# Optimization experiments

Hardware: AMD Instinct MI355X
Metric: run time of the kernel (lower is better)

Reference implementation:

```python
import jax, jax.numpy as jnp
import numpy as np

B, S, D = 2, 2048, 1024
H, HD = 16, 64  # head_dim = D // H
NEG = -9.0e15


def setup_inputs() -> dict:
    key = jax.random.key(0)
    ks = jax.random.split(key, 6)
    # xavier-uniform-like init for projections
    lim_qkv = float(np.sqrt(6.0 / (D + 3 * D)))
    lim_o = float(np.sqrt(6.0 / (D + D)))
    x = jax.random.normal(ks[0], (B, S, D), dtype=jnp.float32)
    qkv_w = jax.random.uniform(ks[1], (3 * D, D), minval=-lim_qkv, maxval=lim_qkv, dtype=jnp.float32)
    qkv_b = jnp.zeros((3 * D,), dtype=jnp.float32)
    o_w = jax.random.uniform(ks[2], (D, D), minval=-lim_o, maxval=lim_o, dtype=jnp.float32)
    o_b = jnp.zeros((D,), dtype=jnp.float32)
    # per-head thresholds ~ Uniform(0, 2/S): mean softmax prob is 1/S, so
    # roughly half the heads prune aggressively, half keep most entries.
    thresholds = jax.random.uniform(ks[3], (H,), dtype=jnp.float32) * (2.0 / S)
    return {"x": x, "thresholds": thresholds, "qkv_w": qkv_w, "qkv_b": qkv_b,
            "o_w": o_w, "o_b": o_b}


def reference(x, thresholds, qkv_w, qkv_b, o_w, o_b):
    # qkv projection: [B,S,3D] -> [B,S,H,3*HD] -> [B,H,S,3*HD]
    qkv = jnp.einsum('bsd,ed->bse', x, qkv_w) + qkv_b
    qkv = qkv.reshape(B, S, H, 3 * HD).transpose(0, 2, 1, 3)
    q, k, v = jnp.split(qkv, 3, axis=-1)  # each [B,H,S,HD]

    scale = 1.0 / jnp.sqrt(jnp.asarray(HD, dtype=q.dtype))
    attn_logits = jnp.einsum('bhqd,bhkd->bhqk', q, k) * scale  # [B,H,S,S]

    # first softmax only to build threshold mask (per-head threshold)
    att1 = jax.nn.softmax(attn_logits, axis=-1)
    mask = att1 > thresholds[None, :, None, None]

    # second, masked softmax
    masked_logits = jnp.where(mask, attn_logits, jnp.asarray(NEG, attn_logits.dtype))
    attention = jax.nn.softmax(masked_logits, axis=-1)

    values = jnp.einsum('bhqk,bhkd->bhqd', attention, v)  # [B,H,S,HD]
    values = values.transpose(0, 2, 1, 3).reshape(B, S, D)
    o = jnp.einsum('bsd,ed->bse', values, o_w) + o_b
    return o
```

## Files before the change

### kernel.cpp

```cpp
#include <hip/hip_runtime.h>
#include <math.h>

#define BATCH 2
#define S_LEN 2048
#define DMODEL 1024
#define NH 16
#define HDIM 64
#define SCALE 0.125f

typedef short bf16x8 __attribute__((ext_vector_type(8)));
typedef _Float16 f16x8 __attribute__((ext_vector_type(8)));
typedef float f32x4 __attribute__((ext_vector_type(4)));
typedef unsigned short u16;
typedef unsigned short u16x4 __attribute__((ext_vector_type(4)));
#define MFMA(a, b, c) __builtin_amdgcn_mfma_f32_16x16x32_bf16(a, b, c, 0, 0, 0)
#define MFMA16(a, b, c) __builtin_amdgcn_mfma_f32_16x16x32_f16(a, b, c, 0, 0, 0)

static __device__ __forceinline__ float bf2f(u16 u) {
  return __uint_as_float(((unsigned int)u) << 16);
}
static __device__ __forceinline__ u16 f2h_bits(float a) {
  _Float16 h = (_Float16)a;
  return *(u16*)&h;
}

static __device__ __forceinline__ void split_bf16(float a, u16& hi, u16& lo) {
  unsigned int u = __float_as_uint(a);
  unsigned int r = (u + 0x7fffu + ((u >> 16) & 1u)) >> 16;
  hi = (u16)r;
  float res = a - __uint_as_float(r << 16);
  unsigned int u2 = __float_as_uint(res);
  lo = (u16)((u2 + 0x7fffu + ((u2 >> 16) & 1u)) >> 16);
}

static __device__ __forceinline__ float qredsum(float v) {
#pragma unroll
  for (int off = 8; off >= 1; off >>= 1) v += __shfl_xor(v, off, 16);
  return v;
}

static __device__ __forceinline__ void async_ld16(u16* lds, const u16* g) {
  __builtin_amdgcn_global_load_lds(
      (const __attribute__((address_space(1))) void*)(const void*)g,
      (__attribute__((address_space(3))) void*)(void*)lds, 16, 0, 0);
}

__global__ __launch_bounds__(256) void split_pair_kernel(
    const float* __restrict__ in, u16* __restrict__ hi, u16* __restrict__ lo,
    int n) {
  int idx = (blockIdx.x * 256 + threadIdx.x) * 4;
  if (idx >= n) return;
  float4 v = *(const float4*)(in + idx);
  u16 h0, h1, h2, h3, l0, l1, l2, l3;
  split_bf16(v.x, h0, l0);
  split_bf16(v.y, h1, l1);
  split_bf16(v.z, h2, l2);
  split_bf16(v.w, h3, l3);
  u16x4 h = {h0, h1, h2, h3};
  u16x4 l = {l0, l1, l2, l3};
  *(u16x4*)(hi + idx) = h;
  *(u16x4*)(lo + idx) = l;
}

__global__ __launch_bounds__(256) void qkv_gemm_mfma(
    const u16* __restrict__ xh, const u16* __restrict__ xl,
    const u16* __restrict__ wh, const u16* __restrict__ wl,
    const float* __restrict__ bias, u16* __restrict__ Qhi,
    u16* __restrict__ Qlo, u16* __restrict__ Khi, u16* __restrict__ Klo,
    u16* __restrict__ Vt) {
  __shared__ __align__(16) u16 Ah[4096], Al[4096], Bh[4096], Bl[4096];
  const int tid = threadIdx.x;
  const int w = tid >> 6, lane = tid & 63;
  const int m = lane & 15, quad = lane >> 4;
  const int wm = w >> 1, wn = w & 1;
  const int m0 = blockIdx.x * 128, n0 = blockIdx.y * 128;
  const int rl = lane >> 2, bp = lane & 3;
  const int sst = (rl >> 1) & 3;
  const int sa = (quad ^ ((m >> 1) & 3)) * 8;

  f32x4 acc[4][4];
  const f32x4 vzero = {0.f, 0.f, 0.f, 0.f};
#pragma unroll
  for (int mt = 0; mt < 4; ++mt)
#pragma unroll
    for (int nt = 0; nt < 4; ++nt) acc[mt][nt] = vzero;

  for (int k0 = 0; k0 < DMODEL; k0 += 32) {
#pragma unroll
    for (int i = 0; i < 2; ++i) {
      int cc = w * 2 + i;
      int row = cc * 16 + rl;
      int gofs = k0 + ((bp ^ sst) << 3);
      async_ld16(&Ah[cc * 512], xh + (m0 + row) * DMODEL + gofs);
      async_ld16(&Al[cc * 512], xl + (m0 + row) * DMODEL + gofs);
      async_ld16(&Bh[cc * 512], wh + (n0 + row) * DMODEL + gofs);
      async_ld16(&Bl[cc * 512], wl + (n0 + row) * DMODEL + gofs);
    }
    __syncthreads();
    bf16x8 afh[4], afl[4], bfh[4], bfl[4];
#pragma unroll
    for (int t = 0; t < 4; ++t) {
      int ra = (wm * 64 + t * 16 + m) * 32 + sa;
      afh[t] = *(const bf16x8*)&Ah[ra];
      afl[t] = *(const bf16x8*)&Al[ra];
      int rb = (wn * 64 + t * 16 + m) * 32 + sa;
      bfh[t] = *(const bf16x8*)&Bh[rb];
      bfl[t] = *(const bf16x8*)&Bl[rb];
    }
#pragma unroll
    for (int mt = 0; mt < 4; ++mt)
#pragma unroll
      for (int nt = 0; nt < 4; ++nt) {
        acc[mt][nt] = MFMA(afh[mt], bfh[nt], acc[mt][nt]);
        acc[mt][nt] = MFMA(afh[mt], bfl[nt], acc[mt][nt]);
        acc[mt][nt] = MFMA(afl[mt], bfh[nt], acc[mt][nt]);
      }
    __syncthreads();
  }
#pragma unroll
  for (int mt = 0; mt < 4; ++mt) {
#pragma unroll
    for (int rg = 0; rg < 4; ++rg) {
      int grow = m0 + wm * 64 + mt * 16 + quad * 4 + rg;
      int bb = grow >> 11, s = grow & (S_LEN - 1);
#pragma unroll
      for (int nt = 0; nt < 4; ++nt) {
        int e = n0 + wn * 64 + nt * 16 + m;
        float val = acc[mt][nt][rg] + bias[e];
        int h = e / 192;
        int r = e - h * 192;
        int d = r & 63;
        int bh = bb * NH + h;
        if (r < 64) {
          u16 hi, lo;
          split_bf16(val, hi, lo);
          int off = (bh * S_LEN + s) * HDIM + d;
          Qhi[off] = hi; Qlo[off] = lo;
        } else if (r < 128) {
          u16 hi, lo;
          split_bf16(val, hi, lo);
          int off = (bh * S_LEN + s) * HDIM + d;
          Khi[off] = hi; Klo[off] = lo;
        } else {
          Vt[(bh * HDIM + d) * S_LEN + s] = f2h_bits(val);
        }
      }
    }
  }
}

__global__ __launch_bounds__(256) void o_gemm_mfma(
    const u16* __restrict__ valh, const u16* __restrict__ vall,
    const float* __restrict__ ow, const float* __restrict__ bias,
    float* __restrict__ out) {
  __shared__ __align__(16) u16 Ah[4096], Al[4096], Bh[4096], Bl[4096];
  const int tid = threadIdx.x;
  const int w = tid >> 6, lane = tid & 63;
  const int m = lane & 15, quad = lane >> 4;
  const int wm = w >> 1, wn = w & 1;
  const int m0 = blockIdx.x * 128, n0 = blockIdx.y * 128;
  const int rl = lane >> 2, bp = lane & 3;
  const int sst = (rl >> 1) & 3;
  const int sa = (quad ^ ((m >> 1) & 3)) * 8;
  const int rB = tid >> 1, hf = tid & 1;
  const int sB = (rB >> 1) & 3;

  f32x4 acc[4][4];
  const f32x4 vzero = {0.f, 0.f, 0.f, 0.f};
#pragma unroll
  for (int mt = 0; mt < 4; ++mt)
#pragma unroll
    for (int nt = 0; nt < 4; ++nt) acc[mt][nt] = vzero;

  for (int k0 = 0; k0 < DMODEL; k0 += 32) {
#pragma unroll
    for (int i = 0; i < 2; ++i) {
      int cc = w * 2 + i;
      int row = cc * 16 + rl;
      int gofs = k0 + ((bp ^ sst) << 3);
      async_ld16(&Ah[cc * 512], valh + (m0 + row) * DMODEL + gofs);
      async_ld16(&Al[cc * 512], vall + (m0 + row) * DMODEL + gofs);
    }
    {
      const float* src = ow + (n0 + rB) * DMODEL + k0 + hf * 16;
      float tmp[16];
      *(float4*)&tmp[0] = *(const float4*)(src);
      *(float4*)&tmp[4] = *(const float4*)(src + 4);
      *(float4*)&tmp[8] = *(const float4*)(src + 8);
      *(float4*)&tmp[12] = *(const float4*)(src + 12);
      u16 hbuf[16], lbuf[16];
#pragma unroll
      for (int ii = 0; ii < 16; ++ii) split_bf16(tmp[ii], hbuf[ii], lbuf[ii]);
#pragma unroll
      for (int j = 0; j < 2; ++j) {
        int bs = ((2 * hf + j) ^ sB) * 8;
        bf16x8 hv, lv;
#pragma unroll
        for (int q2 = 0; q2 < 8; ++q2) {
          hv[q2] = (short)hbuf[j * 8 + q2];
          lv[q2] = (short)lbuf[j * 8 + q2];
        }
        *(bf16x8*)&Bh[rB * 32 + bs] = hv;
        *(bf16x8*)&Bl[rB * 32 + bs] = lv;
      }
    }
    __syncthreads();
    bf16x8 afh[4], afl[4], bfh[4], bfl[4];
#pragma unroll
    for (int t = 0; t < 4; ++t) {
      int ra = (wm * 64 + t * 16 + m) * 32 + sa;
      afh[t] = *(const bf16x8*)&Ah[ra];
      afl[t] = *(const bf16x8*)&Al[ra];
      int rb = (wn * 64 + t * 16 + m) * 32 + sa;
      bfh[t] = *(const bf16x8*)&Bh[rb];
      bfl[t] = *(const bf16x8*)&Bl[rb];
    }
#pragma unroll
    for (int mt = 0; mt < 4; ++mt)
#pragma unroll
      for (int nt = 0; nt < 4; ++nt) {
        acc[mt][nt] = MFMA(afh[mt], bfh[nt], acc[mt][nt]);
        acc[mt][nt] = MFMA(afh[mt], bfl[nt], acc[mt][nt]);
        acc[mt][nt] = MFMA(afl[mt], bfh[nt], acc[mt][nt]);
      }
    __syncthreads();
  }
#pragma unroll
  for (int mt = 0; mt < 4; ++mt) {
#pragma unroll
    for (int rg = 0; rg < 4; ++rg) {
      int grow = m0 + wm * 64 + mt * 16 + quad * 4 + rg;
#pragma unroll
      for (int nt = 0; nt < 4; ++nt) {
        int e = n0 + wn * 64 + nt * 16 + m;
        out[(size_t)grow * DMODEL + e] = acc[mt][nt][rg] + bias[e];
      }
    }
  }
}

__global__ __launch_bounds__(256) void vsum_kernel(const u16* __restrict__ Vt,
                                                   float* __restrict__ vsum) {
  const int bh = blockIdx.x;
  const int tid = threadIdx.x;
  const int d = tid >> 2, part = tid & 3;
  int base = (bh * HDIM + d) * S_LEN + part * 512;
  float s = 0.f;
  for (int k = 0; k < 512; k += 8) {
    f16x8 vv = *(const f16x8*)(Vt + base + k);
#pragma unroll
    for (int j = 0; j < 8; ++j) s += (float)vv[j];
  }
  __shared__ float red[64][4];
  red[d][part] = s;
  __syncthreads();
  if (part == 0)
    vsum[bh * HDIM + d] = red[d][0] + red[d][1] + red[d][2] + red[d][3];
}

__global__ __launch_bounds__(256) void attn_mfma_kernel(
    const u16* __restrict__ Qhi, const u16* __restrict__ Qlo,
    const u16* __restrict__ Khi, const u16* __restrict__ Klo,
    const u16* __restrict__ Vt, const float* __restrict__ thr,
    const float* __restrict__ vsum, u16* __restrict__ valh,
    u16* __restrict__ vall) {
  const int blk = blockIdx.x;
  const int qt = blk & 31, bh = blk >> 5;
  const int h = bh & (NH - 1), bb = bh >> 4;
  const int tid = threadIdx.x;
  const int w = tid >> 6, lane = tid & 63;
  const int m = lane & 15, quad = lane >> 4;
  const int rsub = lane >> 3;
  const int bsw = (lane & 7) ^ rsub;

  __shared__ __align__(16) u16 Kh_s[2][4096];
  __shared__ __align__(16) u16 Kl_s[2][4096];
  __shared__ __align__(16) u16 Vs_s[4096];
  __shared__ __align__(16) u16 Pf_s[4][16][64];

  const int qoff = (bh * S_LEN + qt * 64 + w * 16 + m) * HDIM + quad * 8;
  const bf16x8 aQh0 = *(const bf16x8*)(Qhi + qoff);
  const bf16x8 aQh1 = *(const bf16x8*)(Qhi + qoff + 32);
  const bf16x8 aQl0 = *(const bf16x8*)(Qlo + qoff);
  const bf16x8 aQl1 = *(const bf16x8*)(Qlo + qoff + 32);

  const u16* KhT = Khi + bh * S_LEN * HDIM;
  const u16* KlT = Klo + bh * S_LEN * HDIM;
  const u16* VtT = Vt + bh * HDIM * S_LEN;
  const float th = thr[h];

  const int s0 = (quad ^ (m & 7)) * 8;
  const int s1 = ((4 + quad) ^ (m & 7)) * 8;

  float Zr[4], Z2r[4], tzr[4];
#pragma unroll
  for (int r = 0; r < 4; ++r) { Zr[r] = 0.f; Z2r[r] = 0.f; }

  const f32x4 vzero = {0.f, 0.f, 0.f, 0.f};

#define STAGE_K(bufi, t)                                                     \
  {                                                                          \
    const u16* gh = KhT + (t) * 64 * 64;                                     \
    const u16* gl = KlT + (t) * 64 * 64;                                     \
    _Pragma("unroll") for (int i = 0; i < 2; ++i) {                          \
      int c = w * 2 + i;                                                     \
      int row = c * 8 + rsub;                                                \
      async_ld16(&Kh_s[bufi][c * 512], gh + row * 64 + bsw * 8);             \
      async_ld16(&Kl_s[bufi][c * 512], gl + row * 64 + bsw * 8);             \
    }                                                                        \
  }
#define STAGE_V(t)                                                           \
  {                                                                          \
    _Pragma("unroll") for (int i = 0; i < 2; ++i) {                          \
      int c = w * 2 + i;                                                     \
      int row = c * 8 + rsub;                                                \
      async_ld16(&Vs_s[c * 512], VtT + row * 2048 + (t) * 64 + bsw * 8);     \
    }                                                                        \
  }

  STAGE_K(0, 0);
  __syncthreads();
  for (int t = 0; t < 32; ++t) {
    const int cur = t & 1;
    if (t < 31) STAGE_K(cur ^ 1, t + 1);
    f32x4 acc[4];
#pragma unroll
    for (int nt = 0; nt < 4; ++nt) acc[nt] = vzero;
#pragma unroll
    for (int nt = 0; nt < 4; ++nt) {
      const int ro = (nt * 16 + m) * 64;
      bf16x8 kh0 = *(const bf16x8*)&Kh_s[cur][ro + s0];
      bf16x8 kh1 = *(const bf16x8*)&Kh_s[cur][ro + s1];
      bf16x8 kl0 = *(const bf16x8*)&Kl_s[cur][ro + s0];
      bf16x8 kl1 = *(const bf16x8*)&Kl_s[cur][ro + s1];
      acc[nt] = MFMA(aQh0, kh0, acc[nt]);
      acc[nt] = MFMA(aQh1, kh1, acc[nt]);
      acc[nt] = MFMA(aQh0, kl0, acc[nt]);
      acc[nt] = MFMA(aQh1, kl1, acc[nt]);
      acc[nt] = MFMA(aQl0, kh0, acc[nt]);
      acc[nt] = MFMA(aQl1, kh1, acc[nt]);
      acc[nt] = MFMA(aQl0, kl0, acc[nt]);
      acc[nt] = MFMA(aQl1, kl1, acc[nt]);
    }
#pragma unroll
    for (int r = 0; r < 4; ++r) {
      Zr[r] += __expf(acc[0][r] * SCALE) + __expf(acc[1][r] * SCALE) +
               __expf(acc[2][r] * SCALE) + __expf(acc[3][r] * SCALE);
    }
    __syncthreads();
  }
#pragma unroll
  for (int r = 0; r < 4; ++r) tzr[r] = th * qredsum(Zr[r]);

  f32x4 oacc[4];
#pragma unroll
  for (int nt = 0; nt < 4; ++nt) oacc[nt] = vzero;

  STAGE_K(0, 0);
  __syncthreads();
  for (int t = 0; t < 32; ++t) {
    const int cur = t & 1;
    STAGE_V(t);
    if (t < 31) STAGE_K(cur ^ 1, t + 1);
    f32x4 acc[4];
#pragma unroll
    for (int nt = 0; nt < 4; ++nt) acc[nt] = vzero;
#pragma unroll
    for (int nt = 0; nt < 4; ++nt) {
      const int ro = (nt * 16 + m) * 64;
      bf16x8 kh0 = *(const bf16x8*)&Kh_s[cur][ro + s0];
      bf16x8 kh1 = *(const bf16x8*)&Kh_s[cur][ro + s1];
      bf16x8 kl0 = *(const bf16x8*)&Kl_s[cur][ro + s0];
      bf16x8 kl1 = *(const bf16x8*)&Kl_s[cur][ro + s1];
      acc[nt] = MFMA(aQh0, kh0, acc[nt]);
      acc[nt] = MFMA(aQh1, kh1, acc[nt]);
      acc[nt] = MFMA(aQh0, kl0, acc[nt]);
      acc[nt] = MFMA(aQh1, kl1, acc[nt]);
      acc[nt] = MFMA(aQl0, kh0, acc[nt]);
      acc[nt] = MFMA(aQl1, kh1, acc[nt]);
      acc[nt] = MFMA(aQl0, kl0, acc[nt]);
      acc[nt] = MFMA(aQl1, kl1, acc[nt]);
    }
#pragma unroll
    for (int r = 0; r < 4; ++r) {
      int row = quad * 4 + r;
      float psum = 0.f;
#pragma unroll
      for (int nt = 0; nt < 4; ++nt) {
        float pu = __expf(acc[nt][r] * SCALE);
        float p = (pu > tzr[r]) ? pu : 0.f;
        _Float16 p16 = (_Float16)p;
        psum += (float)p16;
        int col = nt * 16 + m;
        int cs = (((col >> 3) ^ (row & 7)) << 3) | (col & 7);
        Pf_s[w][row][cs] = *(u16*)&p16;
      }
      Z2r[r] += psum;
    }
    __syncthreads();
    f16x8 aP0 = *(const f16x8*)&Pf_s[w][m][s0];
    f16x8 aP1 = *(const f16x8*)&Pf_s[w][m][s1];
#pragma unroll
    for (int nt = 0; nt < 4; ++nt) {
      const int ro = (nt * 16 + m) * 64;
      f16x8 vv0 = *(const f16x8*)&Vs_s[ro + s0];
      f16x8 vv1 = *(const f16x8*)&Vs_s[ro + s1];
      oacc[nt] = MFMA16(aP0, vv0, oacc[nt]);
      oacc[nt] = MFMA16(aP1, vv1, oacc[nt]);
    }
    __syncthreads();
  }

#pragma unroll
  for (int r = 0; r < 4; ++r) {
    float z2 = qredsum(Z2r[r]);
    float invz = (z2 > 0.f) ? (1.f / z2) : 0.f;
    int srow = qt * 64 + w * 16 + quad * 4 + r;
#pragma unroll
    for (int nt = 0; nt < 4; ++nt) {
      float vs = vsum[bh * HDIM + nt * 16 + m];
      float o = (z2 > 0.f) ? (oacc[nt][r] * invz) : (vs * (1.0f / S_LEN));
      int idx = (bb * S_LEN + srow) * DMODEL + h * HDIM + nt * 16 + m;
      u16 hi, lo;
      split_bf16(o, hi, lo);
      valh[idx] = hi;
      vall[idx] = lo;
    }
  }
}

extern "C" void kernel_launch(void* const* d_in, const int* in_sizes, int n_in,
                              void* d_out, int out_size, void* d_ws, size_t ws_size,
                              hipStream_t stream) {
  const float* x = (const float*)d_in[0];
  const float* thresholds = (const float*)d_in[1];
  const float* qkv_w = (const float*)d_in[2];
  const float* qkv_b = (const float*)d_in[3];
  const float* o_w = (const float*)d_in[4];
  const float* o_b = (const float*)d_in[5];

  const size_t NBH = (size_t)BATCH * NH * S_LEN * HDIM;
  u16* base = (u16*)d_ws;
  u16* Qhi = base;
  u16* Qlo = base + NBH;
  u16* Khi = base + 2 * NBH;
  u16* Klo = base + 3 * NBH;
  u16* Vt = base + 4 * NBH;
  float* vsum = (float*)(base + 5 * NBH);
  u16* R1 = (u16*)(vsum + 2048);
  u16* xh = R1;
  u16* xl = R1 + NBH;
  u16* valh = R1;
  u16* vall = R1 + NBH;
  u16* wh = (u16*)d_out;
  u16* wl = wh + (size_t)3 * DMODEL * DMODEL;

  split_pair_kernel<<<4096, 256, 0, stream>>>(x, xh, xl, (int)NBH);
  split_pair_kernel<<<3072, 256, 0, stream>>>(qkv_w, wh, wl, 3 * DMODEL * DMODEL);
  dim3 g1(32, 24);
  qkv_gemm_mfma<<<g1, 256, 0, stream>>>(xh, xl, wh, wl, qkv_b, Qhi, Qlo, Khi,
                                        Klo, Vt);
  vsum_kernel<<<BATCH * NH, 256, 0, stream>>>(Vt, vsum);
  attn_mfma_kernel<<<BATCH * NH * (S_LEN / 64), 256, 0, stream>>>(
      Qhi, Qlo, Khi, Klo, Vt, thresholds, vsum, valh, vall);
  dim3 g3(32, 8);
  o_gemm_mfma<<<g3, 256, 0, stream>>>(valh, vall, o_w, o_b, (float*)d_out);
}
```

Before: 437.9 us.

## Fuse bf16 splitting into QKV GEMM, trim QK MFMAs, double-buffer V

Removes the separate hi/lo split kernels by converting x and qkv_w to bf16 pairs while staging tiles inside the QKV GEMM, sharing a helper with the output GEMM. In attention, the lo*lo QK product terms are dropped, V tiles are double-buffered and prefetched with K, and a block barrier before the P·V step is removed. exp is replaced with exp2 using a folded scale constant. This cuts kernel launches, workspace traffic and MFMA count, at the cost of synchronous loads in the GEMM staging and slightly lower QK precision.

```diff
diff --git a/kernel.cpp b/kernel.cpp
--- a/kernel.cpp
+++ b/kernel.cpp
@@ -7,12 +7,12 @@
 #define NH 16
 #define HDIM 64
 #define SCALE 0.125f
+#define KC 0.18033688011112042f
 
 typedef short bf16x8 __attribute__((ext_vector_type(8)));
 typedef _Float16 f16x8 __attribute__((ext_vector_type(8)));
 typedef float f32x4 __attribute__((ext_vector_type(4)));
 typedef unsigned short u16;
-typedef unsigned short u16x4 __attribute__((ext_vector_type(4)));
 #define MFMA(a, b, c) __builtin_amdgcn_mfma_f32_16x16x32_bf16(a, b, c, 0, 0, 0)
 #define MFMA16(a, b, c) __builtin_amdgcn_mfma_f32_16x16x32_f16(a, b, c, 0, 0, 0)
 
@@ -45,26 +45,33 @@
       (__attribute__((address_space(3))) void*)(void*)lds, 16, 0, 0);
 }
 
-__global__ __launch_bounds__(256) void split_pair_kernel(
-    const float* __restrict__ in, u16* __restrict__ hi, u16* __restrict__ lo,
-    int n) {
-  int idx = (blockIdx.x * 256 + threadIdx.x) * 4;
-  if (idx >= n) return;
-  float4 v = *(const float4*)(in + idx);
-  u16 h0, h1, h2, h3, l0, l1, l2, l3;
-  split_bf16(v.x, h0, l0);
-  split_bf16(v.y, h1, l1);
-  split_bf16(v.z, h2, l2);
-  split_bf16(v.w, h3, l3);
-  u16x4 h = {h0, h1, h2, h3};
-  u16x4 l = {l0, l1, l2, l3};
-  *(u16x4*)(hi + idx) = h;
-  *(u16x4*)(lo + idx) = l;
+static __device__ __forceinline__ void stage_split16(
+    const float* __restrict__ src, u16* __restrict__ Lh, u16* __restrict__ Ll,
+    int r, int hf, int ssw) {
+  float tmp[16];
+  *(float4*)&tmp[0] = *(const float4*)(src);
+  *(float4*)&tmp[4] = *(const float4*)(src + 4);
+  *(float4*)&tmp[8] = *(const float4*)(src + 8);
+  *(float4*)&tmp[12] = *(const float4*)(src + 12);
+  u16 hbuf[16], lbuf[16];
+#pragma unroll
+  for (int ii = 0; ii < 16; ++ii) split_bf16(tmp[ii], hbuf[ii], lbuf[ii]);
+#pragma unroll
+  for (int j = 0; j < 2; ++j) {
+    int bs = ((2 * hf + j) ^ ssw) * 8;
+    bf16x8 hv, lv;
+#pragma unroll
+    for (int q2 = 0; q2 < 8; ++q2) {
+      hv[q2] = (short)hbuf[j * 8 + q2];
+      lv[q2] = (short)lbuf[j * 8 + q2];
+    }
+    *(bf16x8*)&Lh[r * 32 + bs] = hv;
+    *(bf16x8*)&Ll[r * 32 + bs] = lv;
+  }
 }
 
 __global__ __launch_bounds__(256) void qkv_gemm_mfma(
-    const u16* __restrict__ xh, const u16* __restrict__ xl,
-    const u16* __restrict__ wh, const u16* __restrict__ wl,
+    const float* __restrict__ x, const float* __restrict__ wg,
     const float* __restrict__ bias, u16* __restrict__ Qhi,
     u16* __restrict__ Qlo, u16* __restrict__ Khi, u16* __restrict__ Klo,
     u16* __restrict__ Vt) {
@@ -74,9 +81,9 @@
   const int m = lane & 15, quad = lane >> 4;
   const int wm = w >> 1, wn = w & 1;
   const int m0 = blockIdx.x * 128, n0 = blockIdx.y * 128;
-  const int rl = lane >> 2, bp = lane & 3;
-  const int sst = (rl >> 1) & 3;
   const int sa = (quad ^ ((m >> 1) & 3)) * 8;
+  const int rS = tid >> 1, hf = tid & 1;
+  const int sS = (rS >> 1) & 3;
 
   f32x4 acc[4][4];
   const f32x4 vzero = {0.f, 0.f, 0.f, 0.f};
@@ -86,16 +93,10 @@
     for (int nt = 0; nt < 4; ++nt) acc[mt][nt] = vzero;
 
   for (int k0 = 0; k0 < DMODEL; k0 += 32) {
-#pragma unroll
-    for (int i = 0; i < 2; ++i) {
-      int cc = w * 2 + i;
-      int row = cc * 16 + rl;
-      int gofs = k0 + ((bp ^ sst) << 3);
-      async_ld16(&Ah[cc * 512], xh + (m0 + row) * DMODEL + gofs);
-      async_ld16(&Al[cc * 512], xl + (m0 + row) * DMODEL + gofs);
-      async_ld16(&Bh[cc * 512], wh + (n0 + row) * DMODEL + gofs);
-      async_ld16(&Bl[cc * 512], wl + (n0 + row) * DMODEL + gofs);
-    }
+    stage_split16(x + (size_t)(m0 + rS) * DMODEL + k0 + hf * 16, Ah, Al, rS,
+                  hf, sS);
+    stage_split16(wg + (size_t)(n0 + rS) * DMODEL + k0 + hf * 16, Bh, Bl, rS,
+                  hf, sS);
     __syncthreads();
     bf16x8 afh[4], afl[4], bfh[4], bfl[4];
 #pragma unroll
@@ -178,32 +179,11 @@
       int cc = w * 2 + i;
       int row = cc * 16 + rl;
       int gofs = k0 + ((bp ^ sst) << 3);
-      async_ld16(&Ah[cc * 512], valh + (m0 + row) * DMODEL + gofs);
-      async_ld16(&Al[cc * 512], vall + (m0 + row) * DMODEL + gofs);
-    }
-    {
-      const float* src = ow + (n0 + rB) * DMODEL + k0 + hf * 16;
-      float tmp[16];
-      *(float4*)&tmp[0] = *(const float4*)(src);
-      *(float4*)&tmp[4] = *(const float4*)(src + 4);
-      *(float4*)&tmp[8] = *(const float4*)(src + 8);
-      *(float4*)&tmp[12] = *(const float4*)(src + 12);
-      u16 hbuf[16], lbuf[16];
-#pragma unroll
-      for (int ii = 0; ii < 16; ++ii) split_bf16(tmp[ii], hbuf[ii], lbuf[ii]);
-#pragma unroll
-      for (int j = 0; j < 2; ++j) {
-        int bs = ((2 * hf + j) ^ sB) * 8;
-        bf16x8 hv, lv;
-#pragma unroll
-        for (int q2 = 0; q2 < 8; ++q2) {
-          hv[q2] = (short)hbuf[j * 8 + q2];
-          lv[q2] = (short)lbuf[j * 8 + q2];
-        }
-        *(bf16x8*)&Bh[rB * 32 + bs] = hv;
-        *(bf16x8*)&Bl[rB * 32 + bs] = lv;
-      }
-    }
+      async_ld16(&Ah[cc * 512], valh + (size_t)(m0 + row) * DMODEL + gofs);
+      async_ld16(&Al[cc * 512], vall + (size_t)(m0 + row) * DMODEL + gofs);
+    }
+    stage_split16(ow + (size_t)(n0 + rB) * DMODEL + k0 + hf * 16, Bh, Bl, rB,
+                  hf, sB);
     __syncthreads();
     bf16x8 afh[4], afl[4], bfh[4], bfl[4];
 #pragma unroll
@@ -275,7 +255,7 @@
 
   __shared__ __align__(16) u16 Kh_s[2][4096];
   __shared__ __align__(16) u16 Kl_s[2][4096];
-  __shared__ __align__(16) u16 Vs_s[4096];
+  __shared__ __align__(16) u16 Vs_s[2][4096];
   __shared__ __align__(16) u16 Pf_s[4][16][64];
 
   const int qoff = (bh * S_LEN + qt * 64 + w * 16 + m) * HDIM + quad * 8;
@@ -309,13 +289,28 @@
       async_ld16(&Kl_s[bufi][c * 512], gl + row * 64 + bsw * 8);             \
     }                                                                        \
   }
-#define STAGE_V(t)                                                           \
+#define STAGE_V(bufi, t)                                                     \
   {                                                                          \
     _Pragma("unroll") for (int i = 0; i < 2; ++i) {                          \
       int c = w * 2 + i;                                                     \
       int row = c * 8 + rsub;                                                \
-      async_ld16(&Vs_s[c * 512], VtT + row * 2048 + (t) * 64 + bsw * 8);     \
+      async_ld16(&Vs_s[bufi][c * 512], VtT + row * 2048 + (t) * 64 + bsw * 8); \
     }                                                                        \
+  }
+
+#define QK_TILE(cur)                                                         \
+  _Pragma("unroll") for (int nt = 0; nt < 4; ++nt) {                         \
+    const int ro = (nt * 16 + m) * 64;                                       \
+    bf16x8 kh0 = *(const bf16x8*)&Kh_s[cur][ro + s0];                        \
+    bf16x8 kh1 = *(const bf16x8*)&Kh_s[cur][ro + s1];                        \
+    bf16x8 kl0 = *(const bf16x8*)&Kl_s[cur][ro + s0];                        \
+    bf16x8 kl1 = *(const bf16x8*)&Kl_s[cur][ro + s1];                        \
+    acc[nt] = MFMA(aQh0, kh0, acc[nt]);                                      \
+    acc[nt] = MFMA(aQh1, kh1, acc[nt]);                                      \
+    acc[nt] = MFMA(aQh0, kl0, acc[nt]);                                      \
+    acc[nt] = MFMA(aQh1, kl1, acc[nt]);                                      \
+    acc[nt] = MFMA(aQl0, kh0, acc[nt]);                                      \
+    acc[nt] = MFMA(aQl1, kh1, acc[nt]);                                      \
   }
 
   STAGE_K(0, 0);
@@ -326,26 +321,11 @@
     f32x4 acc[4];
 #pragma unroll
     for (int nt = 0; nt < 4; ++nt) acc[nt] = vzero;
-#pragma unroll
-    for (int nt = 0; nt < 4; ++nt) {
-      const int ro = (nt * 16 + m) * 64;
-      bf16x8 kh0 = *(const bf16x8*)&Kh_s[cur][ro + s0];
-      bf16x8 kh1 = *(const bf16x8*)&Kh_s[cur][ro + s1];
-      bf16x8 kl0 = *(const bf16x8*)&Kl_s[cur][ro + s0];
-      bf16x8 kl1 = *(const bf16x8*)&Kl_s[cur][ro + s1];
-      acc[nt] = MFMA(aQh0, kh0, acc[nt]);
-      acc[nt] = MFMA(aQh1, kh1, acc[nt]);
-      acc[nt] = MFMA(aQh0, kl0, acc[nt]);
-      acc[nt] = MFMA(aQh1, kl1, acc[nt]);
-      acc[nt] = MFMA(aQl0, kh0, acc[nt]);
-      acc[nt] = MFMA(aQl1, kh1, acc[nt]);
-      acc[nt] = MFMA(aQl0, kl0, acc[nt]);
-      acc[nt] = MFMA(aQl1, kl1, acc[nt]);
-    }
+    QK_TILE(cur);
 #pragma unroll
     for (int r = 0; r < 4; ++r) {
-      Zr[r] += __expf(acc[0][r] * SCALE) + __expf(acc[1][r] * SCALE) +
-               __expf(acc[2][r] * SCALE) + __expf(acc[3][r] * SCALE);
+      Zr[r] += __builtin_exp2f(acc[0][r] * KC) + __builtin_exp2f(acc[1][r] * KC) +
+               __builtin_exp2f(acc[2][r] * KC) + __builtin_exp2f(acc[3][r] * KC);
     }
     __syncthreads();
   }
@@ -357,37 +337,25 @@
   for (int nt = 0; nt < 4; ++nt) oacc[nt] = vzero;
 
   STAGE_K(0, 0);
+  STAGE_V(0, 0);
   __syncthreads();
   for (int t = 0; t < 32; ++t) {
     const int cur = t & 1;
-    STAGE_V(t);
-    if (t < 31) STAGE_K(cur ^ 1, t + 1);
+    if (t < 31) {
+      STAGE_K(cur ^ 1, t + 1);
+      STAGE_V(cur ^ 1, t + 1);
+    }
     f32x4 acc[4];
 #pragma unroll
     for (int nt = 0; nt < 4; ++nt) acc[nt] = vzero;
-#pragma unroll
-    for (int nt = 0; nt < 4; ++nt) {
-      const int ro = (nt * 16 + m) * 64;
-      bf16x8 kh0 = *(const bf16x8*)&Kh_s[cur][ro + s0];
-      bf16x8 kh1 = *(const bf16x8*)&Kh_s[cur][ro + s1];
-      bf16x8 kl0 = *(const bf16x8*)&Kl_s[cur][ro + s0];
-      bf16x8 kl1 = *(const bf16x8*)&Kl_s[cur][ro + s1];
-      acc[nt] = MFMA(aQh0, kh0, acc[nt]);
-      acc[nt] = MFMA(aQh1, kh1, acc[nt]);
-      acc[nt] = MFMA(aQh0, kl0, acc[nt]);
-      acc[nt] = MFMA(aQh1, kl1, acc[nt]);
-      acc[nt] = MFMA(aQl0, kh0, acc[nt]);
-      acc[nt] = MFMA(aQl1, kh1, acc[nt]);
-      acc[nt] = MFMA(aQl0, kl0, acc[nt]);
-      acc[nt] = MFMA(aQl1, kl1, acc[nt]);
-    }
+    QK_TILE(cur);
 #pragma unroll
     for (int r = 0; r < 4; ++r) {
       int row = quad * 4 + r;
       float psum = 0.f;
 #pragma unroll
       for (int nt = 0; nt < 4; ++nt) {
-        float pu = __expf(acc[nt][r] * SCALE);
+        float pu = __builtin_exp2f(acc[nt][r] * KC);
         float p = (pu > tzr[r]) ? pu : 0.f;
         _Float16 p16 = (_Float16)p;
         psum += (float)p16;
@@ -397,14 +365,13 @@
       }
       Z2r[r] += psum;
     }
-    __syncthreads();
     f16x8 aP0 = *(const f16x8*)&Pf_s[w][m][s0];
     f16x8 aP1 = *(const f16x8*)&Pf_s[w][m][s1];
 #pragma unroll
     for (int nt = 0; nt < 4; ++nt) {
       const int ro = (nt * 16 + m) * 64;
-      f16x8 vv0 = *(const f16x8*)&Vs_s[ro + s0];
-      f16x8 vv1 = *(const f16x8*)&Vs_s[ro + s1];
+      f16x8 vv0 = *(const f16x8*)&Vs_s[cur][ro + s0];
+      f16x8 vv1 = *(const f16x8*)&Vs_s[cur][ro + s1];
       oacc[nt] = MFMA16(aP0, vv0, oacc[nt]);
       oacc[nt] = MFMA16(aP1, vv1, oacc[nt]);
     }
@@ -447,19 +414,12 @@
   u16* Klo = base + 3 * NBH;
   u16* Vt = base + 4 * NBH;
   float* vsum = (float*)(base + 5 * NBH);
-  u16* R1 = (u16*)(vsum + 2048);
-  u16* xh = R1;
-  u16* xl = R1 + NBH;
-  u16* valh = R1;
-  u16* vall = R1 + NBH;
-  u16* wh = (u16*)d_out;
-  u16* wl = wh + (size_t)3 * DMODEL * DMODEL;
-
-  split_pair_kernel<<<4096, 256, 0, stream>>>(x, xh, xl, (int)NBH);
-  split_pair_kernel<<<3072, 256, 0, stream>>>(qkv_w, wh, wl, 3 * DMODEL * DMODEL);
+  u16* valh = (u16*)(vsum + 2048);
+  u16* vall = valh + NBH;
+
   dim3 g1(32, 24);
-  qkv_gemm_mfma<<<g1, 256, 0, stream>>>(xh, xl, wh, wl, qkv_b, Qhi, Qlo, Khi,
-                                        Klo, Vt);
+  qkv_gemm_mfma<<<g1, 256, 0, stream>>>(x, qkv_w, qkv_b, Qhi, Qlo, Khi, Klo,
+                                        Vt);
   vsum_kernel<<<BATCH * NH, 256, 0, stream>>>(Vt, vsum);
   attn_mfma_kernel<<<BATCH * NH * (S_LEN / 64), 256, 0, stream>>>(
       Qhi, Qlo, Khi, Klo, Vt, thresholds, vsum, valh, vall);
```

Result: slower. 495.5 us (+13.1%).
